# Performance work log

Measured on AMD Instinct MI355X. Metric: run time of the kernel, lower is better.

## Reference

```python
import jax, jax.numpy as jnp
import numpy as np

B = 16384
IN = 512
H = 512

def setup_inputs() -> dict:
    key = jax.random.key(0)
    ks = jax.random.split(key, 8)
    inp = {
        "x_t": jax.random.normal(ks[0], (B, IN), dtype=jnp.float32),
        "h_t": jax.random.normal(ks[1], (B, H), dtype=jnp.float32),
        "W_ir": jax.random.normal(ks[2], (IN, H), dtype=jnp.float32),
        "W_hr": jax.random.normal(ks[3], (H, H), dtype=jnp.float32),
        "b_r": jnp.zeros((H,), dtype=jnp.float32),
        "W_iz": jax.random.normal(ks[4], (IN, H), dtype=jnp.float32),
        "W_hz": jax.random.normal(ks[5], (H, H), dtype=jnp.float32),
        "b_z": jnp.zeros((H,), dtype=jnp.float32),
        "W_in": jax.random.normal(ks[6], (IN, H), dtype=jnp.float32),
        "W_hn": jax.random.normal(ks[7], (H, H), dtype=jnp.float32),
        "b_n": jnp.zeros((H,), dtype=jnp.float32),
    }
    return inp

def reference(x_t, h_t, W_ir, W_hr, b_r, W_iz, W_hz, b_z, W_in, W_hn, b_n):
    # Fuse the three input-side and three hidden-side GEMMs by concatenating weights.
    Wi = jnp.concatenate([W_ir, W_iz, W_in], axis=1)   # [IN, 3H]
    Wh = jnp.concatenate([W_hr, W_hz, W_hn], axis=1)   # [H, 3H]
    gi = x_t @ Wi                                      # [B, 3H]
    gh = h_t @ Wh                                      # [B, 3H]
    h = b_r.shape[0]
    r_t = jax.nn.sigmoid(gi[:, :h] + gh[:, :h] + b_r)
    z_t = jax.nn.sigmoid(gi[:, h:2*h] + gh[:, h:2*h] + b_z)
    n_t = jnp.tanh(gi[:, 2*h:] + r_t * gh[:, 2*h:] + b_n)
    return (1.0 - z_t) * n_t + z_t * h_t
```

## Files before the change

### kernel.cpp

```cpp
#include <hip/hip_runtime.h>
#include <hip/hip_fp16.h>

typedef _Float16 half8 __attribute__((ext_vector_type(8)));
typedef float floatx4 __attribute__((ext_vector_type(4)));

#define WLO_OFF (6 * 512 * 512)
#define WSTRIDE ((size_t)(8 * 16 * 2048))

__global__ __launch_bounds__(256) void permute_w(
    const float* __restrict__ Wir, const float* __restrict__ Whr,
    const float* __restrict__ Wiz, const float* __restrict__ Whz,
    const float* __restrict__ Win, const float* __restrict__ Whn,
    _Float16* __restrict__ wperm) {
  __shared__ __align__(16) float tile[32 * 68];
  const int b = blockIdx.x;
  const int w = b >> 7;
  const int rem = b & 127;
  const int ki = rem >> 3;
  const int nt = rem & 7;
  const float* W = (w == 0) ? Wir : (w == 1) ? Whr : (w == 2) ? Wiz
                 : (w == 3) ? Whz : (w == 4) ? Win : Whn;
  const int k0 = ki * 32, n0 = nt * 64;
  const int t = threadIdx.x;

  const int kk = t >> 3;
  const int nn = (t & 7) * 8;
  const float* src = W + (k0 + kk) * 512 + n0 + nn;
  float4 f0 = *(const float4*)(src);
  float4 f1 = *(const float4*)(src + 4);
  float* drow = tile + kk * 68 + nn;
  *(float4*)(drow) = f0;
  *(float4*)(drow + 4) = f1;
  __syncthreads();

  const int u = t >> 6, l = t & 63;
  const int nloc = 16 * u + (l & 15);
  const int kbase = 8 * (l >> 4);
  half8 vh, vl;
#pragma unroll
  for (int j = 0; j < 8; ++j) {
    float f = tile[(kbase + j) * 68 + nloc];
    _Float16 hiv = (_Float16)f;
    vh[j] = hiv;
    vl[j] = (_Float16)(f - (float)hiv);
  }
  const size_t off = ((size_t)((w * 8 + nt) * 16 + ki)) * 2048 + t * 8;
  *(half8*)(wperm + off) = vh;
  *(half8*)(wperm + WLO_OFF + off) = vl;
}

__device__ __forceinline__ void cvt_hilo(const float4 a, const float4 b,
                                         half8& hi, half8& lo) {
  const float v[8] = {a.x, a.y, a.z, a.w, b.x, b.y, b.z, b.w};
#pragma unroll
  for (int j = 0; j < 8; ++j) {
    _Float16 hv = (_Float16)v[j];
    hi[j] = hv;
    lo[j] = (_Float16)(v[j] - (float)hv);
  }
}

__global__ __launch_bounds__(256, 2) void gru_fused(
    const float* __restrict__ x, const float* __restrict__ h,
    const _Float16* __restrict__ wperm,
    const float* __restrict__ br, const float* __restrict__ bz,
    const float* __restrict__ bn, float* __restrict__ out) {
  __shared__ __align__(16) _Float16 ldsXh[4096];
  __shared__ __align__(16) _Float16 ldsXl[4096];
  __shared__ __align__(16) _Float16 ldsHh[4096];
  __shared__ __align__(16) _Float16 ldsHl[4096];

  const int t = threadIdx.x;
  const int lane = t & 63;
  const int wv = t >> 6;
  const int wm = wv >> 1;
  const int wn = wv & 1;
  const int bid = blockIdx.x;
  const int xcd = bid & 7;
  const int uu = bid >> 3;
  const int nt = uu & 7;
  const int mt = ((uu >> 3) << 3) | xcd;
  const int m0 = mt * 128;
  const int n0 = nt * 64;
  const _Float16* whi = wperm;
  const _Float16* wlo = wperm + WLO_OFF;

  floatx4 acc_r[4][2] = {};
  floatx4 acc_z[4][2] = {};
  floatx4 acc_in[4][2] = {};
  floatx4 acc_hn[4][2] = {};

  const int c0 = t, c1 = t + 256;
  const int l0 = c0 & 63, l1 = c1 & 63;
  const int mA0 = 16 * (c0 >> 6) + (l0 & 15), kA0 = 8 * (l0 >> 4);
  const int mA1 = 16 * (c1 >> 6) + (l1 & 15), kA1 = 8 * (l1 >> 4);
  const float* pxb0 = x + (size_t)(m0 + mA0) * 512 + kA0;
  const float* pxb1 = x + (size_t)(m0 + mA1) * 512 + kA1;
  const float* phb0 = h + (size_t)(m0 + mA0) * 512 + kA0;
  const float* phb1 = h + (size_t)(m0 + mA1) * 512 + kA1;

  half8 sth[4], stl[4];
  cvt_hilo(*(const float4*)pxb0, *(const float4*)(pxb0 + 4), sth[0], stl[0]);
  cvt_hilo(*(const float4*)pxb1, *(const float4*)(pxb1 + 4), sth[1], stl[1]);
  cvt_hilo(*(const float4*)phb0, *(const float4*)(phb0 + 4), sth[2], stl[2]);
  cvt_hilo(*(const float4*)phb1, *(const float4*)(phb1 + 4), sth[3], stl[3]);

  for (int kt = 0; kt < 16; ++kt) {
    __syncthreads();
    *(half8*)(ldsXh + c0 * 8) = sth[0];
    *(half8*)(ldsXh + c1 * 8) = sth[1];
    *(half8*)(ldsHh + c0 * 8) = sth[2];
    *(half8*)(ldsHh + c1 * 8) = sth[3];
    *(half8*)(ldsXl + c0 * 8) = stl[0];
    *(half8*)(ldsXl + c1 * 8) = stl[1];
    *(half8*)(ldsHl + c0 * 8) = stl[2];
    *(half8*)(ldsHl + c1 * 8) = stl[3];
    __syncthreads();

    const int kn = ((kt + 1) & 15) * 32;
    float4 nx0 = *(const float4*)(pxb0 + kn);
    float4 nx1 = *(const float4*)(pxb0 + kn + 4);
    float4 nx2 = *(const float4*)(pxb1 + kn);
    float4 nx3 = *(const float4*)(pxb1 + kn + 4);
    float4 nh0 = *(const float4*)(phb0 + kn);
    float4 nh1 = *(const float4*)(phb0 + kn + 4);
    float4 nh2 = *(const float4*)(phb1 + kn);
    float4 nh3 = *(const float4*)(phb1 + kn + 4);

    half8 axh[4], ahh[4];
#pragma unroll
    for (int i = 0; i < 4; ++i) {
      axh[i] = *(const half8*)(ldsXh + ((wm * 4 + i) * 64 + lane) * 8);
      ahh[i] = *(const half8*)(ldsHh + ((wm * 4 + i) * 64 + lane) * 8);
    }
#pragma unroll
    for (int jn = 0; jn < 2; ++jn) {
      const int bo = (wn * 2 + jn) * 512 + lane * 8;
      const size_t tb = ((size_t)(nt * 16 + kt)) * 2048 + bo;
      half8 bh_ir = *(const half8*)(whi + tb + 0 * WSTRIDE);
      half8 bh_hr = *(const half8*)(whi + tb + 1 * WSTRIDE);
      half8 bh_iz = *(const half8*)(whi + tb + 2 * WSTRIDE);
      half8 bh_hz = *(const half8*)(whi + tb + 3 * WSTRIDE);
      half8 bh_in = *(const half8*)(whi + tb + 4 * WSTRIDE);
      half8 bh_hn = *(const half8*)(whi + tb + 5 * WSTRIDE);
#pragma unroll
      for (int i = 0; i < 4; ++i) {
        half8 axl = *(const half8*)(ldsXl + ((wm * 4 + i) * 64 + lane) * 8);
        half8 ahl = *(const half8*)(ldsHl + ((wm * 4 + i) * 64 + lane) * 8);
        acc_r[i][jn]  = __builtin_amdgcn_mfma_f32_16x16x32_f16(axh[i], bh_ir, acc_r[i][jn], 0, 0, 0);
        acc_r[i][jn]  = __builtin_amdgcn_mfma_f32_16x16x32_f16(axl,    bh_ir, acc_r[i][jn], 0, 0, 0);
        acc_r[i][jn]  = __builtin_amdgcn_mfma_f32_16x16x32_f16(ahh[i], bh_hr, acc_r[i][jn], 0, 0, 0);
        acc_r[i][jn]  = __builtin_amdgcn_mfma_f32_16x16x32_f16(ahl,    bh_hr, acc_r[i][jn], 0, 0, 0);
        acc_z[i][jn]  = __builtin_amdgcn_mfma_f32_16x16x32_f16(axh[i], bh_iz, acc_z[i][jn], 0, 0, 0);
        acc_z[i][jn]  = __builtin_amdgcn_mfma_f32_16x16x32_f16(axl,    bh_iz, acc_z[i][jn], 0, 0, 0);
        acc_z[i][jn]  = __builtin_amdgcn_mfma_f32_16x16x32_f16(ahh[i], bh_hz, acc_z[i][jn], 0, 0, 0);
        acc_z[i][jn]  = __builtin_amdgcn_mfma_f32_16x16x32_f16(ahl,    bh_hz, acc_z[i][jn], 0, 0, 0);
        acc_in[i][jn] = __builtin_amdgcn_mfma_f32_16x16x32_f16(axh[i], bh_in, acc_in[i][jn], 0, 0, 0);
        acc_in[i][jn] = __builtin_amdgcn_mfma_f32_16x16x32_f16(axl,    bh_in, acc_in[i][jn], 0, 0, 0);
        acc_hn[i][jn] = __builtin_amdgcn_mfma_f32_16x16x32_f16(ahh[i], bh_hn, acc_hn[i][jn], 0, 0, 0);
        acc_hn[i][jn] = __builtin_amdgcn_mfma_f32_16x16x32_f16(ahl,    bh_hn, acc_hn[i][jn], 0, 0, 0);
      }
      half8 bl_ir = *(const half8*)(wlo + tb + 0 * WSTRIDE);
      half8 bl_hr = *(const half8*)(wlo + tb + 1 * WSTRIDE);
      half8 bl_iz = *(const half8*)(wlo + tb + 2 * WSTRIDE);
      half8 bl_hz = *(const half8*)(wlo + tb + 3 * WSTRIDE);
      half8 bl_in = *(const half8*)(wlo + tb + 4 * WSTRIDE);
      half8 bl_hn = *(const half8*)(wlo + tb + 5 * WSTRIDE);
#pragma unroll
      for (int i = 0; i < 4; ++i) {
        acc_r[i][jn]  = __builtin_amdgcn_mfma_f32_16x16x32_f16(axh[i], bl_ir, acc_r[i][jn], 0, 0, 0);
        acc_r[i][jn]  = __builtin_amdgcn_mfma_f32_16x16x32_f16(ahh[i], bl_hr, acc_r[i][jn], 0, 0, 0);
        acc_z[i][jn]  = __builtin_amdgcn_mfma_f32_16x16x32_f16(axh[i], bl_iz, acc_z[i][jn], 0, 0, 0);
        acc_z[i][jn]  = __builtin_amdgcn_mfma_f32_16x16x32_f16(ahh[i], bl_hz, acc_z[i][jn], 0, 0, 0);
        acc_in[i][jn] = __builtin_amdgcn_mfma_f32_16x16x32_f16(axh[i], bl_in, acc_in[i][jn], 0, 0, 0);
        acc_hn[i][jn] = __builtin_amdgcn_mfma_f32_16x16x32_f16(ahh[i], bl_hn, acc_hn[i][jn], 0, 0, 0);
      }
    }

    cvt_hilo(nx0, nx1, sth[0], stl[0]);
    cvt_hilo(nx2, nx3, sth[1], stl[1]);
    cvt_hilo(nh0, nh1, sth[2], stl[2]);
    cvt_hilo(nh2, nh3, sth[3], stl[3]);
  }

  const int quad = lane >> 4;
  const int col = lane & 15;
#pragma unroll
  for (int i = 0; i < 4; ++i) {
    const int mbase = m0 + wm * 64 + i * 16 + quad * 4;
#pragma unroll
    for (int jn = 0; jn < 2; ++jn) {
      const int n = n0 + wn * 32 + jn * 16 + col;
      const float vbr = br[n], vbz = bz[n], vbn = bn[n];
#pragma unroll
      for (int r = 0; r < 4; ++r) {
        const int m = mbase + r;
        const float gr = acc_r[i][jn][r] + vbr;
        const float gz = acc_z[i][jn][r] + vbz;
        const float rg = 1.0f / (1.0f + __expf(-gr));
        const float zg = 1.0f / (1.0f + __expf(-gz));
        const float gn = acc_in[i][jn][r] + rg * acc_hn[i][jn][r] + vbn;
        const float e2 = __expf(2.0f * gn);
        const float ntv = 1.0f - 2.0f / (e2 + 1.0f);
        const float hp = h[(size_t)m * 512 + n];
        out[(size_t)m * 512 + n] = (1.0f - zg) * ntv + zg * hp;
      }
    }
  }
}

extern "C" void kernel_launch(void* const* d_in, const int* in_sizes, int n_in,
                              void* d_out, int out_size, void* d_ws, size_t ws_size,
                              hipStream_t stream) {
  const float* x   = (const float*)d_in[0];
  const float* h   = (const float*)d_in[1];
  const float* Wir = (const float*)d_in[2];
  const float* Whr = (const float*)d_in[3];
  const float* br  = (const float*)d_in[4];
  const float* Wiz = (const float*)d_in[5];
  const float* Whz = (const float*)d_in[6];
  const float* bz  = (const float*)d_in[7];
  const float* Win = (const float*)d_in[8];
  const float* Whn = (const float*)d_in[9];
  const float* bn  = (const float*)d_in[10];
  float* out = (float*)d_out;
  _Float16* wperm = (_Float16*)d_ws;

  permute_w<<<768, 256, 0, stream>>>(Wir, Whr, Wiz, Whz, Win, Whn, wperm);
  gru_fused<<<1024, 256, 0, stream>>>(x, h, wperm, br, bz, bn, out);
}
```

Measured before the change: 294.9 us.

## Load activation fragments directly from global memory, eliminating LDS staging and barriers

Each wave now reads its x and h fragments directly from global memory and converts them to hi/lo fp16 in registers. This removes the shared-memory tiles and the per-iteration block barriers. The low-weight MFMA pass is split into a separate loop after the high-weight pass. The cost is duplicate global loads across the two column waves, no software prefetch of the next k-tile, and higher register pressure from holding the low parts.

```diff
diff --git a/kernel.cpp b/kernel.cpp
--- a/kernel.cpp
+++ b/kernel.cpp
@@ -65,11 +65,6 @@
     const _Float16* __restrict__ wperm,
     const float* __restrict__ br, const float* __restrict__ bz,
     const float* __restrict__ bn, float* __restrict__ out) {
-  __shared__ __align__(16) _Float16 ldsXh[4096];
-  __shared__ __align__(16) _Float16 ldsXl[4096];
-  __shared__ __align__(16) _Float16 ldsHh[4096];
-  __shared__ __align__(16) _Float16 ldsHl[4096];
-
   const int t = threadIdx.x;
   const int lane = t & 63;
   const int wv = t >> 6;
@@ -85,54 +80,36 @@
   const _Float16* whi = wperm;
   const _Float16* wlo = wperm + WLO_OFF;
 
+  const int mrow = lane & 15;
+  const int koff = 8 * (lane >> 4);
+  const float* pax[4];
+  const float* pah[4];
+#pragma unroll
+  for (int i = 0; i < 4; ++i) {
+    const size_t roff = (size_t)(m0 + wm * 64 + i * 16 + mrow) * 512 + koff;
+    pax[i] = x + roff;
+    pah[i] = h + roff;
+  }
+
   floatx4 acc_r[4][2] = {};
   floatx4 acc_z[4][2] = {};
   floatx4 acc_in[4][2] = {};
   floatx4 acc_hn[4][2] = {};
 
-  const int c0 = t, c1 = t + 256;
-  const int l0 = c0 & 63, l1 = c1 & 63;
-  const int mA0 = 16 * (c0 >> 6) + (l0 & 15), kA0 = 8 * (l0 >> 4);
-  const int mA1 = 16 * (c1 >> 6) + (l1 & 15), kA1 = 8 * (l1 >> 4);
-  const float* pxb0 = x + (size_t)(m0 + mA0) * 512 + kA0;
-  const float* pxb1 = x + (size_t)(m0 + mA1) * 512 + kA1;
-  const float* phb0 = h + (size_t)(m0 + mA0) * 512 + kA0;
-  const float* phb1 = h + (size_t)(m0 + mA1) * 512 + kA1;
-
-  half8 sth[4], stl[4];
-  cvt_hilo(*(const float4*)pxb0, *(const float4*)(pxb0 + 4), sth[0], stl[0]);
-  cvt_hilo(*(const float4*)pxb1, *(const float4*)(pxb1 + 4), sth[1], stl[1]);
-  cvt_hilo(*(const float4*)phb0, *(const float4*)(phb0 + 4), sth[2], stl[2]);
-  cvt_hilo(*(const float4*)phb1, *(const float4*)(phb1 + 4), sth[3], stl[3]);
-
   for (int kt = 0; kt < 16; ++kt) {
-    __syncthreads();
-    *(half8*)(ldsXh + c0 * 8) = sth[0];
-    *(half8*)(ldsXh + c1 * 8) = sth[1];
-    *(half8*)(ldsHh + c0 * 8) = sth[2];
-    *(half8*)(ldsHh + c1 * 8) = sth[3];
-    *(half8*)(ldsXl + c0 * 8) = stl[0];
-    *(half8*)(ldsXl + c1 * 8) = stl[1];
-    *(half8*)(ldsHl + c0 * 8) = stl[2];
-    *(half8*)(ldsHl + c1 * 8) = stl[3];
-    __syncthreads();
-
-    const int kn = ((kt + 1) & 15) * 32;
-    float4 nx0 = *(const float4*)(pxb0 + kn);
-    float4 nx1 = *(const float4*)(pxb0 + kn + 4);
-    float4 nx2 = *(const float4*)(pxb1 + kn);
-    float4 nx3 = *(const float4*)(pxb1 + kn + 4);
-    float4 nh0 = *(const float4*)(phb0 + kn);
-    float4 nh1 = *(const float4*)(phb0 + kn + 4);
-    float4 nh2 = *(const float4*)(phb1 + kn);
-    float4 nh3 = *(const float4*)(phb1 + kn + 4);
-
-    half8 axh[4], ahh[4];
+    const int kb = kt * 32;
+
+    half8 axh[4], axl[4], ahh[4], ahl[4];
 #pragma unroll
     for (int i = 0; i < 4; ++i) {
-      axh[i] = *(const half8*)(ldsXh + ((wm * 4 + i) * 64 + lane) * 8);
-      ahh[i] = *(const half8*)(ldsHh + ((wm * 4 + i) * 64 + lane) * 8);
-    }
+      float4 a0 = *(const float4*)(pax[i] + kb);
+      float4 a1 = *(const float4*)(pax[i] + kb + 4);
+      float4 b0 = *(const float4*)(pah[i] + kb);
+      float4 b1 = *(const float4*)(pah[i] + kb + 4);
+      cvt_hilo(a0, a1, axh[i], axl[i]);
+      cvt_hilo(b0, b1, ahh[i], ahl[i]);
+    }
+
 #pragma unroll
     for (int jn = 0; jn < 2; ++jn) {
       const int bo = (wn * 2 + jn) * 512 + lane * 8;
@@ -145,21 +122,25 @@
       half8 bh_hn = *(const half8*)(whi + tb + 5 * WSTRIDE);
 #pragma unroll
       for (int i = 0; i < 4; ++i) {
-        half8 axl = *(const half8*)(ldsXl + ((wm * 4 + i) * 64 + lane) * 8);
-        half8 ahl = *(const half8*)(ldsHl + ((wm * 4 + i) * 64 + lane) * 8);
         acc_r[i][jn]  = __builtin_amdgcn_mfma_f32_16x16x32_f16(axh[i], bh_ir, acc_r[i][jn], 0, 0, 0);
-        acc_r[i][jn]  = __builtin_amdgcn_mfma_f32_16x16x32_f16(axl,    bh_ir, acc_r[i][jn], 0, 0, 0);
+        acc_r[i][jn]  = __builtin_amdgcn_mfma_f32_16x16x32_f16(axl[i], bh_ir, acc_r[i][jn], 0, 0, 0);
         acc_r[i][jn]  = __builtin_amdgcn_mfma_f32_16x16x32_f16(ahh[i], bh_hr, acc_r[i][jn], 0, 0, 0);
-        acc_r[i][jn]  = __builtin_amdgcn_mfma_f32_16x16x32_f16(ahl,    bh_hr, acc_r[i][jn], 0, 0, 0);
+        acc_r[i][jn]  = __builtin_amdgcn_mfma_f32_16x16x32_f16(ahl[i], bh_hr, acc_r[i][jn], 0, 0, 0);
         acc_z[i][jn]  = __builtin_amdgcn_mfma_f32_16x16x32_f16(axh[i], bh_iz, acc_z[i][jn], 0, 0, 0);
-        acc_z[i][jn]  = __builtin_amdgcn_mfma_f32_16x16x32_f16(axl,    bh_iz, acc_z[i][jn], 0, 0, 0);
+        acc_z[i][jn]  = __builtin_amdgcn_mfma_f32_16x16x32_f16(axl[i], bh_iz, acc_z[i][jn], 0, 0, 0);
         acc_z[i][jn]  = __builtin_amdgcn_mfma_f32_16x16x32_f16(ahh[i], bh_hz, acc_z[i][jn], 0, 0, 0);
-        acc_z[i][jn]  = __builtin_amdgcn_mfma_f32_16x16x32_f16(ahl,    bh_hz, acc_z[i][jn], 0, 0, 0);
+        acc_z[i][jn]  = __builtin_amdgcn_mfma_f32_16x16x32_f16(ahl[i], bh_hz, acc_z[i][jn], 0, 0, 0);
         acc_in[i][jn] = __builtin_amdgcn_mfma_f32_16x16x32_f16(axh[i], bh_in, acc_in[i][jn], 0, 0, 0);
-        acc_in[i][jn] = __builtin_amdgcn_mfma_f32_16x16x32_f16(axl,    bh_in, acc_in[i][jn], 0, 0, 0);
+        acc_in[i][jn] = __builtin_amdgcn_mfma_f32_16x16x32_f16(axl[i], bh_in, acc_in[i][jn], 0, 0, 0);
         acc_hn[i][jn] = __builtin_amdgcn_mfma_f32_16x16x32_f16(ahh[i], bh_hn, acc_hn[i][jn], 0, 0, 0);
-        acc_hn[i][jn] = __builtin_amdgcn_mfma_f32_16x16x32_f16(ahl,    bh_hn, acc_hn[i][jn], 0, 0, 0);
+        acc_hn[i][jn] = __builtin_amdgcn_mfma_f32_16x16x32_f16(ahl[i], bh_hn, acc_hn[i][jn], 0, 0, 0);
       }
+    }
+
+#pragma unroll
+    for (int jn = 0; jn < 2; ++jn) {
+      const int bo = (wn * 2 + jn) * 512 + lane * 8;
+      const size_t tb = ((size_t)(nt * 16 + kt)) * 2048 + bo;
       half8 bl_ir = *(const half8*)(wlo + tb + 0 * WSTRIDE);
       half8 bl_hr = *(const half8*)(wlo + tb + 1 * WSTRIDE);
       half8 bl_iz = *(const half8*)(wlo + tb + 2 * WSTRIDE);
@@ -176,11 +157,6 @@
         acc_hn[i][jn] = __builtin_amdgcn_mfma_f32_16x16x32_f16(ahh[i], bl_hn, acc_hn[i][jn], 0, 0, 0);
       }
     }
-
-    cvt_hilo(nx0, nx1, sth[0], stl[0]);
-    cvt_hilo(nx2, nx3, sth[1], stl[1]);
-    cvt_hilo(nh0, nh1, sth[2], stl[2]);
-    cvt_hilo(nh2, nh3, sth[3], stl[3]);
   }
 
   const int quad = lane >> 4;
```

After: 435.7 us. 1.48x slower.
